# Kernel optimization log

Hardware: AMD Instinct MI355X
Metric: run time of the kernel (lower is better)

The kernel has to match this reference:

```python
import jax, jax.numpy as jnp
import numpy as np

N_AGENTS, DEG, F_DIM, H_DIM, OUT_DIM = 4096, 32, 256, 256, 128
RATIO = 0.2  # SAGPooling ratio hardcoded in NeighNet


def _build_matrix():
    # circulant adjacency: agent i linked to i+1..i+DEG (mod N), constant degree
    i = np.repeat(np.arange(N_AGENTS), DEG)
    j = (np.arange(N_AGENTS)[:, None] + np.arange(1, DEG + 1)[None, :]) % N_AGENTS
    mat = np.zeros((N_AGENTS, N_AGENTS), np.int32)
    mat[i, j.reshape(-1)] = 1
    return mat


def setup_inputs():
    key = jax.random.key(0)
    ks = jax.random.split(key, 8)
    h4 = H_DIM // 4
    w = lambda k, shape, fan: (jax.random.normal(k, shape, jnp.float32) / np.sqrt(fan))
    return {
        "data": jax.random.normal(ks[0], (N_AGENTS, F_DIM), jnp.float32),
        "matrix": jnp.asarray(_build_matrix()),
        "W1c": w(ks[1], (F_DIM, h4), F_DIM), "b1c": jnp.zeros((h4,), jnp.float32),
        "W2c": w(ks[2], (h4, H_DIM), h4), "b2c": jnp.zeros((H_DIM,), jnp.float32),
        "Wrel": w(ks[3], (H_DIM, 1), H_DIM), "brel": jnp.zeros((1,), jnp.float32),
        "Wroot": w(ks[4], (H_DIM, 1), H_DIM),
        "Wl1": w(ks[5], (2 * H_DIM, H_DIM), 2 * H_DIM), "bl1": jnp.zeros((H_DIM,), jnp.float32),
        "Wl2": w(ks[6], (H_DIM, OUT_DIM), H_DIM), "bl2": jnp.zeros((OUT_DIM,), jnp.float32),
    }


def _get_neigh_indices(mat):
    # host-side (like original .cpu()/nonzero loop), but vectorized numpy
    mat = np.asarray(jax.device_get(mat))
    n = mat.shape[-1]
    counts = (mat != 0).sum(-1)                         # n_neigh per agent
    _, cols = np.nonzero(mat)                            # row-major: grouped by agent
    total = int(n + counts.sum())
    starts = np.concatenate([[0], np.cumsum(counts + 1)])[:-1]  # center node position per subgraph
    gather_idx = np.empty(total, np.int64)
    gather_idx[starts] = np.arange(n)                    # center = agent's own data
    m = np.ones(total, bool); m[starts] = False
    gather_idx[m] = cols                                 # neighbors follow center, in row order
    e0 = np.concatenate([[0], np.cumsum(counts)])[:-1]
    rank = np.arange(int(counts.sum())) - np.repeat(e0, counts)
    nei = np.repeat(starts, counts) + rank + 1           # global ids of neighbor nodes
    ctr = np.repeat(starts, counts)
    src = np.concatenate([ctr, nei])                     # center->neigh and neigh->center
    dst = np.concatenate([nei, ctr])
    return gather_idx, src, dst, total, n


def _gcn(x, W, b, src, dst, n):
    # PyG GCNConv: lin -> add self loops -> D^-1/2 (A+I) D^-1/2 aggregation -> +bias
    h = x @ W
    loop = jnp.arange(n)
    s = jnp.concatenate([src, loop])
    d = jnp.concatenate([dst, loop])
    deg = jax.ops.segment_sum(jnp.ones(s.shape[0], x.dtype), d, num_segments=n)
    dinv = jnp.where(deg > 0, jax.lax.rsqrt(jnp.where(deg > 0, deg, 1.0)), 0.0)
    msg = (dinv[s] * dinv[d])[:, None] * h[s]
    return jax.ops.segment_sum(msg, d, num_segments=n) + b


def reference(data, matrix, W1c, b1c, W2c, b2c, Wrel, brel, Wroot, Wl1, bl1, Wl2, bl2):
    gather_np, src_np, dst_np, total, n = _get_neigh_indices(matrix)
    G = total // n                       # uniform subgraph size (constant degree)
    k = int(np.ceil(RATIO * G))          # SAGPooling keeps ceil(ratio*G) nodes
    gather_idx = jnp.asarray(gather_np)
    src = jnp.asarray(src_np); dst = jnp.asarray(dst_np)

    x = data[gather_idx]                                  # [total, F]
    x = jax.nn.relu(_gcn(x, W1c, b1c, src, dst, total))   # [total, H/4]
    x = jax.nn.relu(_gcn(x, W2c, b2c, src, dst, total))   # [total, H]

    # SAGPooling: GraphConv score (sum-aggr neighbors @ Wrel + b + x @ Wroot), tanh gate, per-graph top-k
    agg = jax.ops.segment_sum(x[src], dst, num_segments=total)
    score = (agg @ Wrel + brel + x @ Wroot)[:, 0]         # [total]
    score_g = score.reshape(n, G)                         # subgraphs are contiguous blocks
    topv, topi = jax.lax.top_k(score_g, k)                # [n, k]
    xg = x.reshape(n, G, -1)
    xk = jnp.take_along_axis(xg, topi[:, :, None], axis=1) * jnp.tanh(topv)[:, :, None]

    # global max pool || global mean pool over kept nodes per graph
    z = jnp.concatenate([xk.max(axis=1), xk.mean(axis=1)], axis=-1)  # [n, 2H]
    return jax.nn.relu(z @ Wl1 + bl1) @ Wl2 + bl2                     # [n, OUT]
```

## Files before the change

### kernel.cpp

```cpp
#include <hip/hip_runtime.h>
#include <math.h>


#define N_AG   4096
#define GSZ    33
#define FDIM   256
#define H4     64
#define HDIM   256
#define ODIM   128
#define KTOP   7
#define SY2LD  260

typedef __attribute__((ext_vector_type(8)))  short short8v;
typedef __attribute__((ext_vector_type(16))) float f32x16;

__device__ __forceinline__ float relu(float x) { return fmaxf(x, 0.f); }

constexpr float A_C = 1.0f / 33.0f;
constexpr float B_C = 0.12309149097933272f;

__device__ __forceinline__ unsigned short bf16_rne(float x) {
  unsigned u = __builtin_bit_cast(unsigned, x);
  return (unsigned short)((u + 0x7FFFu + ((u >> 16) & 1u)) >> 16);
}
__device__ __forceinline__ float bf16_to_f(unsigned short h) {
  return __builtin_bit_cast(float, (unsigned)h << 16);
}

__global__ __launch_bounds__(64) void k_feat(const float* __restrict__ data,
                                             const float* __restrict__ W1c,
                                             float* __restrict__ Hb) {
  __shared__ float sd[FDIM];
  const int i = blockIdx.x, c = threadIdx.x;
  for (int k = c; k < FDIM; k += 64) sd[k] = data[i * FDIM + k];
  __syncthreads();
  float acc = 0.f;
#pragma unroll
  for (int k4 = 0; k4 < FDIM / 4; ++k4) {
    const float4 dv = *reinterpret_cast<const float4*>(&sd[k4 * 4]);
    acc += dv.x * W1c[(k4 * 4 + 0) * H4 + c];
    acc += dv.y * W1c[(k4 * 4 + 1) * H4 + c];
    acc += dv.z * W1c[(k4 * 4 + 2) * H4 + c];
    acc += dv.w * W1c[(k4 * 4 + 3) * H4 + c];
  }
  Hb[i * H4 + c] = acc;
}

__global__ __launch_bounds__(256, 3) void k_sub(
    const float* __restrict__ Hb,  const float* __restrict__ b1c,
    const float* __restrict__ W2c, const float* __restrict__ b2c,
    const float* __restrict__ Wrel, const float* __restrict__ brel,
    const float* __restrict__ Wroot, float* __restrict__ Zb) {
  __shared__ float sy2f[GSZ * SY2LD];
  __shared__ unsigned short x1h[32 * 64];
  __shared__ unsigned short x1l[32 * 64];
  __shared__ float x1r32[64];
  __shared__ float sred[4][64];
  __shared__ float srel[GSZ], sroot[GSZ], ssc[GSZ], stanv[KTOP];
  __shared__ int   ssel[KTOP];

  const int i = blockIdx.x, t = threadIdx.x;
  const int lane = t & 63, wid = t >> 6;
  const int m5 = lane & 31, hg = lane >> 5;

  short8v Bh[2][4], Bl[2][4];
#pragma unroll
  for (int tile = 0; tile < 2; ++tile) {
    const int n = wid * 64 + tile * 32 + m5;
#pragma unroll
    for (int ks = 0; ks < 4; ++ks) {
      short8v vh, vl;
#pragma unroll
      for (int j = 0; j < 8; ++j) {
        const float w = W2c[(ks * 16 + 8 * hg + j) * HDIM + n];
        const unsigned short hb = bf16_rne(w);
        vh[j] = (short)hb;
        vl[j] = (short)bf16_rne(w - bf16_to_f(hb));
      }
      Bh[tile][ks] = vh; Bl[tile][ks] = vl;
    }
  }

  {
    const int c = t & 63, rg = t >> 6;
    const float hc = Hb[i * H4 + c];
    const float b1 = b1c[c];
    float hm[8]; float part = 0.f;
#pragma unroll
    for (int m = 0; m < 8; ++m) {
      hm[m] = Hb[(size_t)((i + 1 + rg + 4 * m) & (N_AG - 1)) * H4 + c];
      part += hm[m];
    }
    sred[rg][c] = part;
#pragma unroll
    for (int m = 0; m < 8; ++m) {
      const int r = 1 + rg + 4 * m;
      const float v = relu(B_C * hc + 0.5f * hm[m] + b1);
      if (r < 32) {
        const int idx = r * 64 + (c ^ ((r & 7) << 3));
        const unsigned short hb = bf16_rne(v);
        x1h[idx] = hb;
        x1l[idx] = bf16_rne(v - bf16_to_f(hb));
      } else {
        x1r32[c] = v;
      }
    }
    __syncthreads();
    if (t < 64) {
      const float s = sred[0][c] + sred[1][c] + sred[2][c] + sred[3][c];
      const float v = relu(A_C * hc + B_C * s + b1);
      const unsigned short hb = bf16_rne(v);
      x1h[c] = hb;
      x1l[c] = bf16_rne(v - bf16_to_f(hb));
    }
    __syncthreads();
  }

  {
    f32x16 acc0, acc1;
#pragma unroll
    for (int r = 0; r < 16; ++r) { acc0[r] = 0.f; acc1[r] = 0.f; }
#pragma unroll
    for (int ks = 0; ks < 4; ++ks) {
      const int es = (ks * 16 + 8 * hg) ^ ((m5 & 7) << 3);
      const short8v ah = *reinterpret_cast<const short8v*>(&x1h[m5 * 64 + es]);
      const short8v al = *reinterpret_cast<const short8v*>(&x1l[m5 * 64 + es]);
      acc0 = __builtin_amdgcn_mfma_f32_32x32x16_bf16(ah, Bh[0][ks], acc0, 0, 0, 0);
      acc0 = __builtin_amdgcn_mfma_f32_32x32x16_bf16(ah, Bl[0][ks], acc0, 0, 0, 0);
      acc0 = __builtin_amdgcn_mfma_f32_32x32x16_bf16(al, Bh[0][ks], acc0, 0, 0, 0);
      acc1 = __builtin_amdgcn_mfma_f32_32x32x16_bf16(ah, Bh[1][ks], acc1, 0, 0, 0);
      acc1 = __builtin_amdgcn_mfma_f32_32x32x16_bf16(ah, Bl[1][ks], acc1, 0, 0, 0);
      acc1 = __builtin_amdgcn_mfma_f32_32x32x16_bf16(al, Bh[1][ks], acc1, 0, 0, 0);
    }
#pragma unroll
    for (int r = 0; r < 16; ++r) {
      const int row = (r & 3) + 8 * (r >> 2) + 4 * hg;
      sy2f[row * SY2LD + wid * 64 + m5]      = acc0[r];
      sy2f[row * SY2LD + wid * 64 + 32 + m5] = acc1[r];
    }
    float a32 = 0.f;
#pragma unroll
    for (int k4 = 0; k4 < 16; ++k4) {
      const float4 xv = *reinterpret_cast<const float4*>(&x1r32[k4 * 4]);
      a32 += xv.x * W2c[(k4 * 4 + 0) * HDIM + t];
      a32 += xv.y * W2c[(k4 * 4 + 1) * HDIM + t];
      a32 += xv.z * W2c[(k4 * 4 + 2) * HDIM + t];
      a32 += xv.w * W2c[(k4 * 4 + 3) * HDIM + t];
    }
    sy2f[32 * SY2LD + t] = a32;
    __syncthreads();
  }

  {
    float hv[GSZ];
#pragma unroll
    for (int r = 0; r < GSZ; ++r) hv[r] = sy2f[r * SY2LD + t];
    float sumn = 0.f;
#pragma unroll
    for (int r = 1; r < GSZ; ++r) sumn += hv[r];
    const float b2 = b2c[t];
    sy2f[t] = relu(A_C * hv[0] + B_C * sumn + b2);
#pragma unroll
    for (int r = 1; r < GSZ; ++r)
      sy2f[r * SY2LD + t] = relu(B_C * hv[0] + 0.5f * hv[r] + b2);
    __syncthreads();
  }

  {
    const float4 wr4 = *reinterpret_cast<const float4*>(&Wrel[lane * 4]);
    const float4 wq4 = *reinterpret_cast<const float4*>(&Wroot[lane * 4]);
    for (int n = wid; n < GSZ; n += 4) {
      const float4 yv = *reinterpret_cast<const float4*>(&sy2f[n * SY2LD + lane * 4]);
      float dr = yv.x * wr4.x + yv.y * wr4.y + yv.z * wr4.z + yv.w * wr4.w;
      float dq = yv.x * wq4.x + yv.y * wq4.y + yv.z * wq4.z + yv.w * wq4.w;
#pragma unroll
      for (int off = 32; off; off >>= 1) {
        dr += __shfl_down(dr, off);
        dq += __shfl_down(dq, off);
      }
      if (lane == 0) { srel[n] = dr; sroot[n] = dq; }
    }
    __syncthreads();
    if (wid == 0) {
      float rv = (lane >= 1 && lane < GSZ) ? srel[lane] : 0.f;
#pragma unroll
      for (int off = 32; off; off >>= 1) rv += __shfl_down(rv, off);
      const float sumrel = __shfl(rv, 0);
      if (lane < GSZ) {
        const float aggdot = (lane == 0) ? sumrel : srel[0];
        ssc[lane] = aggdot + brel[0] + sroot[lane];
      }
    }
    __syncthreads();
  }

  if (wid == 0) {
    float v = (lane < GSZ) ? ssc[lane] : -INFINITY;
#pragma unroll
    for (int it = 0; it < KTOP; ++it) {
      float bv = v; int bi = lane;
#pragma unroll
      for (int off = 32; off; off >>= 1) {
        const float ov = __shfl_xor(bv, off);
        const int   oi = __shfl_xor(bi, off);
        if (ov > bv || (ov == bv && oi < bi)) { bv = ov; bi = oi; }
      }
      if (lane == 0) { ssel[it] = bi; stanv[it] = tanhf(bv); }
      if (lane == bi) v = -INFINITY;
    }
  }
  __syncthreads();

  {
    float mx = -INFINITY, sm = 0.f;
#pragma unroll
    for (int m = 0; m < KTOP; ++m) {
      const float val = sy2f[ssel[m] * SY2LD + t] * stanv[m];
      mx = fmaxf(mx, val);
      sm += val;
    }
    Zb[(size_t)i * (2 * HDIM) + t] = mx;
    Zb[(size_t)i * (2 * HDIM) + HDIM + t] = sm * (1.0f / 7.0f);
  }
}

__global__ __launch_bounds__(256) void k_mlp(
    const float* __restrict__ Zb,  const float* __restrict__ Wl1,
    const float* __restrict__ bl1, const float* __restrict__ Wl2,
    const float* __restrict__ bl2, float* __restrict__ out) {
  __shared__ float sz[16][2 * HDIM];
  __shared__ float su[16][HDIM];
  const int b = blockIdx.x, t = threadIdx.x;
  const int row0 = b * 16;
  for (int idx = t; idx < 16 * 2 * HDIM; idx += 256)
    (&sz[0][0])[idx] = Zb[(size_t)row0 * (2 * HDIM) + idx];
  __syncthreads();

  float acc[16];
#pragma unroll
  for (int r = 0; r < 16; ++r) acc[r] = 0.f;
  for (int k4 = 0; k4 < (2 * HDIM) / 4; ++k4) {
    const float w0 = Wl1[(k4 * 4 + 0) * HDIM + t];
    const float w1 = Wl1[(k4 * 4 + 1) * HDIM + t];
    const float w2 = Wl1[(k4 * 4 + 2) * HDIM + t];
    const float w3 = Wl1[(k4 * 4 + 3) * HDIM + t];
#pragma unroll
    for (int r = 0; r < 16; ++r) {
      const float4 zv = *reinterpret_cast<const float4*>(&sz[r][k4 * 4]);
      acc[r] += zv.x * w0 + zv.y * w1 + zv.z * w2 + zv.w * w3;
    }
  }
  const float b1 = bl1[t];
#pragma unroll
  for (int r = 0; r < 16; ++r) su[r][t] = relu(acc[r] + b1);
  __syncthreads();

  const int c2 = t & 127, rh = t >> 7;
  float a2[8];
#pragma unroll
  for (int r = 0; r < 8; ++r) a2[r] = 0.f;
  for (int k4 = 0; k4 < HDIM / 4; ++k4) {
    const float w0 = Wl2[(k4 * 4 + 0) * ODIM + c2];
    const float w1 = Wl2[(k4 * 4 + 1) * ODIM + c2];
    const float w2 = Wl2[(k4 * 4 + 2) * ODIM + c2];
    const float w3 = Wl2[(k4 * 4 + 3) * ODIM + c2];
#pragma unroll
    for (int r = 0; r < 8; ++r) {
      const float4 uv = *reinterpret_cast<const float4*>(&su[rh * 8 + r][k4 * 4]);
      a2[r] += uv.x * w0 + uv.y * w1 + uv.z * w2 + uv.w * w3;
    }
  }
  const float b2 = bl2[c2];
#pragma unroll
  for (int r = 0; r < 8; ++r)
    out[(size_t)(row0 + rh * 8 + r) * ODIM + c2] = a2[r] + b2;
}

extern "C" void kernel_launch(void* const* d_in, const int* in_sizes, int n_in,
                              void* d_out, int out_size, void* d_ws, size_t ws_size,
                              hipStream_t stream) {
  const float* data  = (const float*)d_in[0];
  const float* W1c   = (const float*)d_in[2];
  const float* b1c   = (const float*)d_in[3];
  const float* W2c   = (const float*)d_in[4];
  const float* b2c   = (const float*)d_in[5];
  const float* Wrel  = (const float*)d_in[6];
  const float* brel  = (const float*)d_in[7];
  const float* Wroot = (const float*)d_in[8];
  const float* Wl1   = (const float*)d_in[9];
  const float* bl1   = (const float*)d_in[10];
  const float* Wl2   = (const float*)d_in[11];
  const float* bl2   = (const float*)d_in[12];
  float* out = (float*)d_out;

  float* Hb = (float*)d_ws;
  float* Zb = Hb + (size_t)N_AG * H4;

  k_feat<<<N_AG, 64, 0, stream>>>(data, W1c, Hb);
  k_sub <<<N_AG, 256, 0, stream>>>(Hb, b1c, W2c, b2c, Wrel, brel, Wroot, Zb);
  k_mlp<<<N_AG / 16, 256, 0, stream>>>(Zb, Wl1, bl1, Wl2, bl2, out);
}
```

Measured before the change: 256.4 us.

## Add weight-transpose prep kernel and use transposed, pre-split weights across kernels

A new prep kernel transposes W1c, W2c, Wl1 and Wl2 into k-contiguous layouts and precomputes the bf16 hi/lo split of W2c once per call. k_sub no longer does that split in every block and loads its MFMA operands as vector reads. k_feat and k_mlp now read the weights as float4 rows, k_feat handles 4 rows per block, and k_mlp's rows per block drop from 16 to 8 to double its block count. The cost is an extra launch plus transposed weights that each thread reads along its own row, so lanes read strided addresses instead of coalesced ones, and k_mlp gets less reuse of each weight load.

```diff
diff --git a/kernel.cpp b/kernel.cpp
--- a/kernel.cpp
+++ b/kernel.cpp
@@ -27,28 +27,64 @@
   return __builtin_bit_cast(float, (unsigned)h << 16);
 }
 
-__global__ __launch_bounds__(64) void k_feat(const float* __restrict__ data,
-                                             const float* __restrict__ W1c,
-                                             float* __restrict__ Hb) {
-  __shared__ float sd[FDIM];
-  const int i = blockIdx.x, c = threadIdx.x;
-  for (int k = c; k < FDIM; k += 64) sd[k] = data[i * FDIM + k];
+__global__ __launch_bounds__(256) void k_prep(
+    const float* __restrict__ W2c, const float* __restrict__ W1c,
+    const float* __restrict__ Wl1, const float* __restrict__ Wl2,
+    unsigned short* __restrict__ W2Th, unsigned short* __restrict__ W2Tl,
+    float* __restrict__ W2Tf, float* __restrict__ W1T,
+    float* __restrict__ Wl1T, float* __restrict__ Wl2T) {
+  const int gid = blockIdx.x * 256 + threadIdx.x;
+  for (int j = gid; j < 196608; j += 65536) {
+    if (j < 16384) {
+      const int k = j >> 8, n = j & 255;
+      const float w = W2c[j];
+      const unsigned short hb = bf16_rne(w);
+      W2Th[n * 64 + k] = hb;
+      W2Tl[n * 64 + k] = bf16_rne(w - bf16_to_f(hb));
+      W2Tf[n * 64 + k] = w;
+    } else if (j < 32768) {
+      const int i2 = j - 16384;
+      const int k = i2 >> 6, c = i2 & 63;
+      W1T[c * 256 + k] = W1c[i2];
+    } else if (j < 163840) {
+      const int i2 = j - 32768;
+      const int k = i2 >> 8, n = i2 & 255;
+      Wl1T[n * 512 + k] = Wl1[i2];
+    } else {
+      const int i2 = j - 163840;
+      const int k = i2 >> 7, n = i2 & 127;
+      Wl2T[n * 256 + k] = Wl2[i2];
+    }
+  }
+}
+
+__global__ __launch_bounds__(256) void k_feat(const float* __restrict__ data,
+                                              const float* __restrict__ W1T,
+                                              float* __restrict__ Hb) {
+  __shared__ float sd[4][FDIM];
+  const int b = blockIdx.x, t = threadIdx.x;
+  const int row0 = b * 4;
+  for (int idx = t; idx < 4 * FDIM; idx += 256)
+    (&sd[0][0])[idx] = data[(size_t)row0 * FDIM + idx];
   __syncthreads();
+  const int r = t >> 6, c = t & 63;
   float acc = 0.f;
 #pragma unroll
   for (int k4 = 0; k4 < FDIM / 4; ++k4) {
-    const float4 dv = *reinterpret_cast<const float4*>(&sd[k4 * 4]);
-    acc += dv.x * W1c[(k4 * 4 + 0) * H4 + c];
-    acc += dv.y * W1c[(k4 * 4 + 1) * H4 + c];
-    acc += dv.z * W1c[(k4 * 4 + 2) * H4 + c];
-    acc += dv.w * W1c[(k4 * 4 + 3) * H4 + c];
-  }
-  Hb[i * H4 + c] = acc;
+    const float4 dv = *reinterpret_cast<const float4*>(&sd[r][k4 * 4]);
+    const float4 wv = *reinterpret_cast<const float4*>(&W1T[c * 256 + k4 * 4]);
+    acc += dv.x * wv.x;
+    acc += dv.y * wv.y;
+    acc += dv.z * wv.z;
+    acc += dv.w * wv.w;
+  }
+  Hb[(row0 + r) * H4 + c] = acc;
 }
 
 __global__ __launch_bounds__(256, 3) void k_sub(
     const float* __restrict__ Hb,  const float* __restrict__ b1c,
-    const float* __restrict__ W2c, const float* __restrict__ b2c,
+    const unsigned short* __restrict__ W2Th, const unsigned short* __restrict__ W2Tl,
+    const float* __restrict__ W2Tf, const float* __restrict__ b2c,
     const float* __restrict__ Wrel, const float* __restrict__ brel,
     const float* __restrict__ Wroot, float* __restrict__ Zb) {
   __shared__ float sy2f[GSZ * SY2LD];
@@ -69,15 +105,8 @@
     const int n = wid * 64 + tile * 32 + m5;
 #pragma unroll
     for (int ks = 0; ks < 4; ++ks) {
-      short8v vh, vl;
-#pragma unroll
-      for (int j = 0; j < 8; ++j) {
-        const float w = W2c[(ks * 16 + 8 * hg + j) * HDIM + n];
-        const unsigned short hb = bf16_rne(w);
-        vh[j] = (short)hb;
-        vl[j] = (short)bf16_rne(w - bf16_to_f(hb));
-      }
-      Bh[tile][ks] = vh; Bl[tile][ks] = vl;
+      Bh[tile][ks] = *reinterpret_cast<const short8v*>(&W2Th[n * 64 + ks * 16 + 8 * hg]);
+      Bl[tile][ks] = *reinterpret_cast<const short8v*>(&W2Tl[n * 64 + ks * 16 + 8 * hg]);
     }
   }
 
@@ -142,10 +171,11 @@
 #pragma unroll
     for (int k4 = 0; k4 < 16; ++k4) {
       const float4 xv = *reinterpret_cast<const float4*>(&x1r32[k4 * 4]);
-      a32 += xv.x * W2c[(k4 * 4 + 0) * HDIM + t];
-      a32 += xv.y * W2c[(k4 * 4 + 1) * HDIM + t];
-      a32 += xv.z * W2c[(k4 * 4 + 2) * HDIM + t];
-      a32 += xv.w * W2c[(k4 * 4 + 3) * HDIM + t];
+      const float4 wv = *reinterpret_cast<const float4*>(&W2Tf[t * 64 + k4 * 4]);
+      a32 += xv.x * wv.x;
+      a32 += xv.y * wv.y;
+      a32 += xv.z * wv.z;
+      a32 += xv.w * wv.w;
     }
     sy2f[32 * SY2LD + t] = a32;
     __syncthreads();
@@ -225,55 +255,49 @@
 }
 
 __global__ __launch_bounds__(256) void k_mlp(
-    const float* __restrict__ Zb,  const float* __restrict__ Wl1,
-    const float* __restrict__ bl1, const float* __restrict__ Wl2,
+    const float* __restrict__ Zb,  const float* __restrict__ Wl1T,
+    const float* __restrict__ bl1, const float* __restrict__ Wl2T,
     const float* __restrict__ bl2, float* __restrict__ out) {
-  __shared__ float sz[16][2 * HDIM];
-  __shared__ float su[16][HDIM];
+  __shared__ float sz[8][2 * HDIM];
+  __shared__ float su[8][HDIM];
   const int b = blockIdx.x, t = threadIdx.x;
-  const int row0 = b * 16;
-  for (int idx = t; idx < 16 * 2 * HDIM; idx += 256)
+  const int row0 = b * 8;
+  for (int idx = t; idx < 8 * 2 * HDIM; idx += 256)
     (&sz[0][0])[idx] = Zb[(size_t)row0 * (2 * HDIM) + idx];
   __syncthreads();
 
-  float acc[16];
-#pragma unroll
-  for (int r = 0; r < 16; ++r) acc[r] = 0.f;
+  float acc[8];
+#pragma unroll
+  for (int r = 0; r < 8; ++r) acc[r] = 0.f;
   for (int k4 = 0; k4 < (2 * HDIM) / 4; ++k4) {
-    const float w0 = Wl1[(k4 * 4 + 0) * HDIM + t];
-    const float w1 = Wl1[(k4 * 4 + 1) * HDIM + t];
-    const float w2 = Wl1[(k4 * 4 + 2) * HDIM + t];
-    const float w3 = Wl1[(k4 * 4 + 3) * HDIM + t];
-#pragma unroll
-    for (int r = 0; r < 16; ++r) {
+    const float4 wv = *reinterpret_cast<const float4*>(&Wl1T[t * 512 + k4 * 4]);
+#pragma unroll
+    for (int r = 0; r < 8; ++r) {
       const float4 zv = *reinterpret_cast<const float4*>(&sz[r][k4 * 4]);
-      acc[r] += zv.x * w0 + zv.y * w1 + zv.z * w2 + zv.w * w3;
+      acc[r] += zv.x * wv.x + zv.y * wv.y + zv.z * wv.z + zv.w * wv.w;
     }
   }
   const float b1 = bl1[t];
 #pragma unroll
-  for (int r = 0; r < 16; ++r) su[r][t] = relu(acc[r] + b1);
+  for (int r = 0; r < 8; ++r) su[r][t] = relu(acc[r] + b1);
   __syncthreads();
 
   const int c2 = t & 127, rh = t >> 7;
-  float a2[8];
-#pragma unroll
-  for (int r = 0; r < 8; ++r) a2[r] = 0.f;
+  float a2[4];
+#pragma unroll
+  for (int r = 0; r < 4; ++r) a2[r] = 0.f;
   for (int k4 = 0; k4 < HDIM / 4; ++k4) {
-    const float w0 = Wl2[(k4 * 4 + 0) * ODIM + c2];
-    const float w1 = Wl2[(k4 * 4 + 1) * ODIM + c2];
-    const float w2 = Wl2[(k4 * 4 + 2) * ODIM + c2];
-    const float w3 = Wl2[(k4 * 4 + 3) * ODIM + c2];
-#pragma unroll
-    for (int r = 0; r < 8; ++r) {
-      const float4 uv = *reinterpret_cast<const float4*>(&su[rh * 8 + r][k4 * 4]);
-      a2[r] += uv.x * w0 + uv.y * w1 + uv.z * w2 + uv.w * w3;
+    const float4 wv = *reinterpret_cast<const float4*>(&Wl2T[c2 * 256 + k4 * 4]);
+#pragma unroll
+    for (int r = 0; r < 4; ++r) {
+      const float4 uv = *reinterpret_cast<const float4*>(&su[rh * 4 + r][k4 * 4]);
+      a2[r] += uv.x * wv.x + uv.y * wv.y + uv.z * wv.z + uv.w * wv.w;
     }
   }
   const float b2 = bl2[c2];
 #pragma unroll
-  for (int r = 0; r < 8; ++r)
-    out[(size_t)(row0 + rh * 8 + r) * ODIM + c2] = a2[r] + b2;
+  for (int r = 0; r < 4; ++r)
+    out[(size_t)(row0 + rh * 4 + r) * ODIM + c2] = a2[r] + b2;
 }
 
 extern "C" void kernel_launch(void* const* d_in, const int* in_sizes, int n_in,
@@ -294,9 +318,18 @@
   float* out = (float*)d_out;
 
   float* Hb = (float*)d_ws;
-  float* Zb = Hb + (size_t)N_AG * H4;
-
-  k_feat<<<N_AG, 64, 0, stream>>>(data, W1c, Hb);
-  k_sub <<<N_AG, 256, 0, stream>>>(Hb, b1c, W2c, b2c, Wrel, brel, Wroot, Zb);
-  k_mlp<<<N_AG / 16, 256, 0, stream>>>(Zb, Wl1, bl1, Wl2, bl2, out);
-}
+  float* Zb = Hb + 262144;
+  unsigned short* W2Th = (unsigned short*)(Zb + 2097152);
+  unsigned short* W2Tl = W2Th + 16384;
+  float* W2Tf = (float*)(W2Tl + 16384);
+  float* W1T  = W2Tf + 16384;
+  float* Wl1T = W1T + 16384;
+  float* Wl2T = Wl1T + 131072;
+
+  k_prep<<<256, 256, 0, stream>>>(W2c, W1c, Wl1, Wl2,
+                                  W2Th, W2Tl, W2Tf, W1T, Wl1T, Wl2T);
+  k_feat<<<N_AG / 4, 256, 0, stream>>>(data, W1T, Hb);
+  k_sub <<<N_AG, 256, 0, stream>>>(Hb, b1c, W2Th, W2Tl, W2Tf, b2c,
+                                   Wrel, brel, Wroot, Zb);
+  k_mlp <<<N_AG / 8, 256, 0, stream>>>(Zb, Wl1T, bl1, Wl2T, bl2, out);
+}
```

Result: slower. 286.2 us (+11.6%).
